# Kernel optimization log

Measured on AMD Instinct MI355X. Metric: run time of the kernel, lower is better.

Reference implementation:

```python
import jax, jax.numpy as jnp
import numpy as np

N_NODES = 100000
N_EDGES = 600000
HID = 128
N_ETYPES = 8


def setup_inputs() -> dict:
    key = jax.random.key(0)
    ks = jax.random.split(key, 10)
    s = 1.0 / np.sqrt(HID)
    return {
        "h": jax.random.normal(ks[0], (N_NODES, HID), dtype=jnp.float32),
        "edge_index": jax.random.randint(ks[1], (2, N_EDGES), 0, N_NODES, dtype=jnp.int64),
        "edge_type": jax.random.randint(ks[2], (N_EDGES,), 0, N_ETYPES, dtype=jnp.int64),
        # per-edge-type Linear(hidden, hidden): weight (T, H_out, H_in) stored as (T, H_in, H_out) for einsum
        "message_W": jax.random.uniform(ks[3], (N_ETYPES, HID, HID), jnp.float32, -s, s),
        "message_b": jax.random.uniform(ks[4], (N_ETYPES, HID), jnp.float32, -s, s),
        # GRUCell params (torch layout): w_ih (3H, H), w_hh (3H, H), b_ih (3H,), b_hh (3H,)
        "gru_w_ih": jax.random.uniform(ks[5], (3 * HID, HID), jnp.float32, -s, s),
        "gru_w_hh": jax.random.uniform(ks[6], (3 * HID, HID), jnp.float32, -s, s),
        "gru_b_ih": jax.random.uniform(ks[7], (3 * HID,), jnp.float32, -s, s),
        "gru_b_hh": jax.random.uniform(ks[8], (3 * HID,), jnp.float32, -s, s),
    }


def reference(h, edge_index, edge_type, message_W, message_b,
              gru_w_ih, gru_w_hh, gru_b_ih, gru_b_hh):
    num_nodes = h.shape[0]
    src, dst = edge_index[0], edge_index[1]

    # Transform every node by every edge-type Linear once: (N, T, H).
    # Equivalent to per-type msg = h[src] @ W[t].T + b[t] gathered by edge type.
    all_msgs = jnp.einsum('nh,thd->ntd', h, message_W) + message_b  # (N, T, H)
    msg = all_msgs[src, edge_type]                                   # (E, H) gather
    messages = jax.ops.segment_sum(msg, dst, num_segments=num_nodes)  # scatter-add

    # GRUCell: r,z,n gates (torch semantics)
    gi = messages @ gru_w_ih.T + gru_b_ih  # (N, 3H)
    gh = h @ gru_w_hh.T + gru_b_hh         # (N, 3H)
    i_r, i_z, i_n = jnp.split(gi, 3, axis=-1)
    h_r, h_z, h_n = jnp.split(gh, 3, axis=-1)
    r = jax.nn.sigmoid(i_r + h_r)
    z = jax.nn.sigmoid(i_z + h_z)
    n = jnp.tanh(i_n + r * h_n)
    return (1.0 - z) * n + z * h
```

## Files before the change

kernel.cpp:

```cpp
#include <hip/hip_runtime.h>

#define HID 128
#define NTY 8

typedef __attribute__((ext_vector_type(8))) short bf16x8;
typedef __attribute__((ext_vector_type(4))) float f32x4;

__device__ __forceinline__ unsigned short f2bf(float x) {
    unsigned u = __float_as_uint(x);
    u += 0x7FFF + ((u >> 16) & 1);
    return (unsigned short)(u >> 16);
}
__device__ __forceinline__ float bf2f(unsigned short s) {
    return __uint_as_float(((unsigned)s) << 16);
}
__device__ __forceinline__ float sigmoidf_fast(float x) {
    return 1.f / (1.f + __expf(-x));
}
__device__ __forceinline__ float tanhf_fast(float x) {
    return 1.f - 2.f / (1.f + __expf(2.f * x));
}

__global__ void conv_all_kernel(const float* __restrict__ h, unsigned short* __restrict__ hbf, int nh,
                                const float* __restrict__ W, unsigned short* __restrict__ wfr,
                                const float* __restrict__ wih, const float* __restrict__ whh,
                                unsigned short* __restrict__ wpkf,
                                int* __restrict__ sortedE, int capE,
                                int* __restrict__ seg8, int M8)
{
    int i = blockIdx.x * 256 + threadIdx.x;
    if (i < nh) { hbf[i] = f2bf(h[i]); return; }
    i -= nh;
    if (i < 131072) {
        int e = i & 7, lane = (i >> 3) & 63, cb = (i >> 9) & 7, kc = (i >> 12) & 3, t = i >> 14;
        int lr = lane & 15, quad = lane >> 4;
        int d = cb * 16 + lr;
        int k = kc * 32 + quad * 8 + e;
        wfr[i] = f2bf(W[(t << 14) + (k << 7) + d]);
        return;
    }
    i -= 131072;
    if (i < 98304) {
        int e = i & 7, lane = (i >> 3) & 63, f = i >> 9;
        int ct = f & 7, fg = f >> 3;
        int g3 = fg % 3, kc = fg / 3;
        int lr = lane & 15, quad = lane >> 4;
        int d = ct * 16 + lr;
        int kk = quad * 8 + e;
        float v;
        if (kc < 4) v = wih[(g3 * 128 + d) * 128 + kc * 32 + kk];
        else        v = whh[(g3 * 128 + d) * 128 + (kc - 4) * 32 + kk];
        wpkf[i] = f2bf(v);
        return;
    }
    i -= 98304;
    if (i < capE) { sortedE[i] = -1; return; }
    i -= capE;
    if (i < M8) seg8[i] = 0;
}

__global__ void hist8_kernel(const int* __restrict__ etype, const int* __restrict__ ei,
                             int E, int N, int* __restrict__ seg8) {
    int stride = gridDim.x * blockDim.x;
    for (int i = blockIdx.x * blockDim.x + threadIdx.x; i < E; i += stride)
        atomicAdd(&seg8[etype[i] * N + ei[E + i]], 1);
}

__global__ void scanA_kernel(int* __restrict__ seg8, int* __restrict__ bsum, int M8) {
    __shared__ int s[256];
    int i = blockIdx.x * 256 + threadIdx.x;
    int v = (i < M8) ? seg8[i] : 0;
    s[threadIdx.x] = v;
    __syncthreads();
    for (int off = 1; off < 256; off <<= 1) {
        int t = (threadIdx.x >= off) ? s[threadIdx.x - off] : 0;
        __syncthreads();
        s[threadIdx.x] += t;
        __syncthreads();
    }
    if (i < M8) seg8[i] = s[threadIdx.x] - v;
    if (threadIdx.x == 255) bsum[blockIdx.x] = s[255];
}

__global__ void scanBbig_kernel(int* __restrict__ bsum, int nb,
                                const int* __restrict__ seg8, int N, int E,
                                int* __restrict__ padB, int* __restrict__ padA) {
    __shared__ int s[256];
    int tx = threadIdx.x;
    int C = (nb + 255) / 256;
    int lo = tx * C, hi = lo + C; if (hi > nb) hi = nb;
    int sum = 0;
    for (int j = lo; j < hi; ++j) sum += bsum[j];
    s[tx] = sum;
    __syncthreads();
    for (int off = 1; off < 256; off <<= 1) {
        int t = (tx >= off) ? s[tx - off] : 0;
        __syncthreads();
        s[tx] += t;
        __syncthreads();
    }
    int run = s[tx] - sum;
    for (int j = lo; j < hi; ++j) { int v = bsum[j]; bsum[j] = run; run += v; }
    __syncthreads();
    if (tx == 0) {
        int r[9];
        for (int t = 0; t < 8; ++t) { int k = t * N; r[t] = seg8[k] + bsum[k >> 8]; }
        r[8] = E;
        int pb = 0;
        for (int t = 0; t < 8; ++t) {
            padB[t] = pb;
            padA[t] = pb - r[t];
            int c = r[t + 1] - r[t];
            pb += (c + 127) & ~127;
        }
        padB[8] = pb;
    }
}

__global__ void scanC_kernel(int* __restrict__ seg8, const int* __restrict__ bsum,
                             const int* __restrict__ padA, int M8, int N) {
    int i = blockIdx.x * 256 + threadIdx.x;
    if (i < M8) {
        int t = i / N;
        seg8[i] += bsum[i >> 8] + padA[t];
    }
}

__global__ void scatter8_kernel(const int* __restrict__ etype, const int* __restrict__ ei,
                                int E, int N, int* __restrict__ seg8, int* __restrict__ sortedE) {
    int stride = gridDim.x * blockDim.x;
    for (int i = blockIdx.x * blockDim.x + threadIdx.x; i < E; i += stride) {
        int pos = atomicAdd(&seg8[etype[i] * N + ei[E + i]], 1);
        sortedE[pos] = ei[i];
    }
}

__global__ __launch_bounds__(256) void msg_gemm(
    const unsigned short* __restrict__ hbf, const unsigned short* __restrict__ wfr,
    const float* __restrict__ bias, const int* __restrict__ sortedE,
    const int* __restrict__ padB, unsigned short* __restrict__ M)
{
    __shared__ unsigned short hs[128][136];
    __shared__ int srcs[128];
    __shared__ int stype;

    int tx = threadIdx.x;
    int base = blockIdx.x * 128;
    if (tx < 128) srcs[tx] = sortedE[base + tx];
    if (tx == 0) {
        int t = -1;
        #pragma unroll
        for (int tt = 0; tt < 8; ++tt)
            if (base >= padB[tt] && base < padB[tt + 1]) t = tt;
        stype = t;
    }
    __syncthreads();
    int t = stype;
    if (t < 0) return;

    for (int f = tx; f < 2048; f += 256) {
        int row = f >> 4, c8 = (f & 15) * 8;
        int s = srcs[row]; if (s < 0) s = 0;
        *(uint4*)&hs[row][c8] = *(const uint4*)&hbf[(size_t)s * 128 + c8];
    }
    __syncthreads();

    int lane = tx & 63, w = tx >> 6;
    int r0 = (w >> 1) * 64, c0 = (w & 1) * 64;
    int lr = lane & 15, quad = lane >> 4;
    f32x4 acc[4][4] = {};

    const unsigned short* wt = wfr + (t << 14) + ((unsigned)(c0 >> 4) << 9) + (lane << 3);
    #pragma unroll
    for (int kc = 0; kc < 4; ++kc) {
        bf16x8 af[4], wf[4];
        #pragma unroll
        for (int rb = 0; rb < 4; ++rb) af[rb] = *(const bf16x8*)&hs[r0 + rb * 16 + lr][kc * 32 + quad * 8];
        #pragma unroll
        for (int cb = 0; cb < 4; ++cb) wf[cb] = *(const bf16x8*)&wt[(kc << 12) + (cb << 9)];
        #pragma unroll
        for (int rb = 0; rb < 4; ++rb)
            #pragma unroll
            for (int cb = 0; cb < 4; ++cb)
                acc[rb][cb] = __builtin_amdgcn_mfma_f32_16x16x32_bf16(wf[cb], af[rb], acc[rb][cb], 0, 0, 0);
    }

    float4 bv4[4];
    #pragma unroll
    for (int cb = 0; cb < 4; ++cb)
        bv4[cb] = *(const float4*)&bias[t * 128 + c0 + cb * 16 + quad * 4];

    #pragma unroll
    for (int rb = 0; rb < 4; ++rb) {
        int e = r0 + rb * 16 + lr;
        size_t mrow = (size_t)(base + e);
        #pragma unroll
        for (int cb = 0; cb < 4; ++cb) {
            int d0 = c0 + cb * 16 + quad * 4;
            f32x4 a = acc[rb][cb];
            uint2 v;
            v.x = (unsigned)f2bf(a[0] + bv4[cb].x) | ((unsigned)f2bf(a[1] + bv4[cb].y) << 16);
            v.y = (unsigned)f2bf(a[2] + bv4[cb].z) | ((unsigned)f2bf(a[3] + bv4[cb].w) << 16);
            *(uint2*)&M[mrow * 128 + d0] = v;
        }
    }
}

__global__ __launch_bounds__(512, 4) void gru_fused(
    const unsigned short* __restrict__ M, const int* __restrict__ segE,
    const int* __restrict__ padB, const unsigned short* __restrict__ hbf,
    const unsigned short* __restrict__ wpkf, const float* __restrict__ bih,
    const float* __restrict__ bhh, const float* __restrict__ hf,
    float* __restrict__ out, int N)
{
    __shared__ unsigned short As[4][2048];
    __shared__ int bnds_l[520];

    int tx = threadIdx.x;
    int n0 = blockIdx.x * 64;

    for (int jl = tx; jl < 520; jl += 512) {
        int t = jl / 65, j = jl - t * 65;
        int nidx = n0 + j - 1;
        int v;
        if (nidx < 0) v = padB[t];
        else {
            if (nidx > N - 1) nidx = N - 1;
            v = segE[t * N + nidx];
        }
        bnds_l[jl] = v;
    }

    int lane = tx & 63, w = tx >> 6;
    int lr = lane & 15, quad = lane >> 4;
    int rt = w & 3, cg = w >> 2;
    int node = n0 + rt * 16 + lr;
    bool valid = node < N;
    int nc = valid ? node : (N - 1);

    bf16x8 afh[4];
    {
        const unsigned short* hrow = hbf + ((size_t)nc << 7) + (quad << 3);
        #pragma unroll
        for (int k4 = 0; k4 < 4; ++k4) afh[k4] = *(const bf16x8*)&hrow[k4 * 32];
    }
    __syncthreads();

    {
        int ln = tx >> 3, j8 = tx & 7;
        float a[16];
        #pragma unroll
        for (int j = 0; j < 16; ++j) a[j] = 0.f;

        int tcur = 0;
        int r = bnds_l[ln], re = bnds_l[ln + 1];
        while (r >= re && tcur < 7) {
            ++tcur;
            r = bnds_l[tcur * 65 + ln];
            re = bnds_l[tcur * 65 + ln + 1];
        }
        bool have = (r < re);
        uint4 c0v, c1v;
        if (have) {
            const unsigned short* p = M + (size_t)r * 128 + j8 * 16;
            c0v = *(const uint4*)p;
            c1v = *(const uint4*)(p + 8);
        }
        while (have) {
            uint4 p0 = c0v, p1 = c1v;
            int rn = r + 1, tn = tcur, ren = re;
            while (rn >= ren && tn < 7) {
                ++tn;
                rn = bnds_l[tn * 65 + ln];
                ren = bnds_l[tn * 65 + ln + 1];
            }
            bool haveN = (rn < ren);
            if (haveN) {
                const unsigned short* p = M + (size_t)rn * 128 + j8 * 16;
                c0v = *(const uint4*)p;
                c1v = *(const uint4*)(p + 8);
            }
            const unsigned short* q0 = (const unsigned short*)&p0;
            const unsigned short* q1 = (const unsigned short*)&p1;
            #pragma unroll
            for (int u = 0; u < 8; ++u) {
                a[u]     += bf2f(q0[u]);
                a[8 + u] += bf2f(q1[u]);
            }
            r = rn; tcur = tn; re = ren; have = haveN;
        }

        unsigned short tmp[16];
        #pragma unroll
        for (int j = 0; j < 16; ++j) tmp[j] = f2bf(a[j]);
        int lrw = ln & 15, wv = ln >> 4;
        int swz = (lrw & 7) << 4;
        int b0 = ((lrw << 8) + (j8 << 5)) ^ swz;
        int b1 = ((lrw << 8) + (j8 << 5) + 16) ^ swz;
        *(uint4*)((char*)&As[wv][0] + b0) = *(const uint4*)&tmp[0];
        *(uint4*)((char*)&As[wv][0] + b1) = *(const uint4*)&tmp[8];
    }
    __syncthreads();

    const unsigned short* AsW = &As[rt][0];
    const unsigned short* wg = wpkf + (lane << 3);

    f32x4 aR[4] = {}, aZ[4] = {}, aI[4] = {}, aH[4] = {};
    #pragma unroll
    for (int kc = 0; kc < 8; ++kc) {
        bf16x8 af;
        if (kc < 4) {
            int byte = ((lr << 8) + (kc << 6) + (quad << 4)) ^ ((lr & 7) << 4);
            af = *(const bf16x8*)((char*)AsW + byte);
        } else {
            af = afh[kc - 4];
        }
        #pragma unroll
        for (int g3 = 0; g3 < 3; ++g3) {
            #pragma unroll
            for (int ct = 0; ct < 4; ++ct) {
                bf16x8 wf = *(const bf16x8*)&wg[(unsigned)((kc * 3 + g3) * 8 + cg * 4 + ct) << 9];
                if (g3 == 0)      aR[ct] = __builtin_amdgcn_mfma_f32_16x16x32_bf16(wf, af, aR[ct], 0, 0, 0);
                else if (g3 == 1) aZ[ct] = __builtin_amdgcn_mfma_f32_16x16x32_bf16(wf, af, aZ[ct], 0, 0, 0);
                else if (kc < 4)  aI[ct] = __builtin_amdgcn_mfma_f32_16x16x32_bf16(wf, af, aI[ct], 0, 0, 0);
                else              aH[ct] = __builtin_amdgcn_mfma_f32_16x16x32_bf16(wf, af, aH[ct], 0, 0, 0);
            }
        }
    }

    if (valid) {
        #pragma unroll
        for (int ct = 0; ct < 4; ++ct) {
            int d0 = cg * 64 + ct * 16 + quad * 4;
            f32x4 bir = *(const f32x4*)&bih[d0],       bhr = *(const f32x4*)&bhh[d0];
            f32x4 biz = *(const f32x4*)&bih[128 + d0], bhz = *(const f32x4*)&bhh[128 + d0];
            f32x4 bin = *(const f32x4*)&bih[256 + d0], bhn = *(const f32x4*)&bhh[256 + d0];
            f32x4 h0 = *(const f32x4*)&hf[(size_t)node * 128 + d0];
            f32x4 o;
            #pragma unroll
            for (int j = 0; j < 4; ++j) {
                float r  = sigmoidf_fast(aR[ct][j] + bir[j] + bhr[j]);
                float z  = sigmoidf_fast(aZ[ct][j] + biz[j] + bhz[j]);
                float nn = tanhf_fast(aI[ct][j] + bin[j] + r * (aH[ct][j] + bhn[j]));
                o[j] = (1.f - z) * nn + z * h0[j];
            }
            *(f32x4*)&out[(size_t)node * 128 + d0] = o;
        }
    }
}

extern "C" void kernel_launch(void* const* d_in, const int* in_sizes, int n_in,
                              void* d_out, int out_size, void* d_ws, size_t ws_size,
                              hipStream_t stream)
{
    const float* h     = (const float*)d_in[0];
    const int*   ei    = (const int*)d_in[1];
    const int*   etype = (const int*)d_in[2];
    const float* W     = (const float*)d_in[3];
    const float* b     = (const float*)d_in[4];
    const float* wih   = (const float*)d_in[5];
    const float* whh   = (const float*)d_in[6];
    const float* bih   = (const float*)d_in[7];
    const float* bhh   = (const float*)d_in[8];
    float* out = (float*)d_out;

    int E = in_sizes[1] / 2;
    int N = in_sizes[0] / HID;
    int M8 = N * 8;
    int nbA = (M8 + 255) / 256;
    int capE = ((E + 127) / 128 + NTY) * 128;

    char* p = (char*)d_ws;
    auto alloc = [&](size_t bytes) { char* r = p; p += (bytes + 255) & ~(size_t)255; return r; };
    unsigned short* hbf  = (unsigned short*)alloc((size_t)N * 128 * 2);
    unsigned short* wfr  = (unsigned short*)alloc((size_t)131072 * 2);
    unsigned short* wpkf = (unsigned short*)alloc((size_t)98304 * 2);
    int* seg8    = (int*)alloc((size_t)M8 * 4);
    int* bsum    = (int*)alloc((size_t)nbA * 4);
    int* sortedE = (int*)alloc((size_t)capE * 4);
    int* padB    = (int*)alloc(9 * 4);
    int* padA    = (int*)alloc(8 * 4);
    unsigned short* M = (unsigned short*)alloc((size_t)capE * 128 * 2);
    (void)ws_size;

    int totalConv = N * 128 + 131072 + 98304 + capE + M8;
    conv_all_kernel<<<(totalConv + 255) / 256, 256, 0, stream>>>(
        h, hbf, N * 128, W, wfr, wih, whh, wpkf, sortedE, capE, seg8, M8);

    hist8_kernel<<<1024, 256, 0, stream>>>(etype, ei, E, N, seg8);
    scanA_kernel<<<nbA, 256, 0, stream>>>(seg8, bsum, M8);
    scanBbig_kernel<<<1, 256, 0, stream>>>(bsum, nbA, seg8, N, E, padB, padA);
    scanC_kernel<<<nbA, 256, 0, stream>>>(seg8, bsum, padA, M8, N);
    scatter8_kernel<<<1024, 256, 0, stream>>>(etype, ei, E, N, seg8, sortedE);

    msg_gemm<<<capE / 128, 256, 0, stream>>>(hbf, wfr, b, sortedE, padB, M);
    gru_fused<<<(N + 63) / 64, 512, 0, stream>>>(M, seg8, padB, hbf, wpkf, bih, bhh, h, out, N);
}
```

Measured before the change: 380.8 us.

## Fuse preprocessing and counting-sort stages into one cooperative kernel with grid syncs

```diff
diff --git a/kernel.cpp b/kernel.cpp
--- a/kernel.cpp
+++ b/kernel.cpp
@@ -1,4 +1,7 @@
 #include <hip/hip_runtime.h>
+#include <hip/hip_cooperative_groups.h>
+
+namespace cg = cooperative_groups;
 
 #define HID 128
 #define NTY 8
@@ -21,26 +24,35 @@
     return 1.f - 2.f / (1.f + __expf(2.f * x));
 }
 
-__global__ void conv_all_kernel(const float* __restrict__ h, unsigned short* __restrict__ hbf, int nh,
-                                const float* __restrict__ W, unsigned short* __restrict__ wfr,
-                                const float* __restrict__ wih, const float* __restrict__ whh,
-                                unsigned short* __restrict__ wpkf,
-                                int* __restrict__ sortedE, int capE,
-                                int* __restrict__ seg8, int M8)
+__global__ __launch_bounds__(256) void prep_sort_coop(
+    const float* __restrict__ h, unsigned short* __restrict__ hbf, int nh,
+    const float* __restrict__ W, unsigned short* __restrict__ wfr,
+    const float* __restrict__ wih, const float* __restrict__ whh,
+    unsigned short* __restrict__ wpkf,
+    const int* __restrict__ ei, const int* __restrict__ etype, int E, int N,
+    int* __restrict__ seg8, int* __restrict__ bsum,
+    int* __restrict__ padB, int* __restrict__ padA,
+    int* __restrict__ sortedE, int capE)
 {
-    int i = blockIdx.x * 256 + threadIdx.x;
-    if (i < nh) { hbf[i] = f2bf(h[i]); return; }
-    i -= nh;
-    if (i < 131072) {
+    cg::grid_group grid = cg::this_grid();
+    __shared__ int s[256];
+
+    int tx = threadIdx.x;
+    int gtid = blockIdx.x * 256 + tx;
+    int gsz = gridDim.x * 256;
+    int nb = gridDim.x;
+    int M8 = N * 8;
+    int CB = (M8 + nb - 1) / nb;
+
+    for (int i = gtid; i < nh; i += gsz) hbf[i] = f2bf(h[i]);
+    for (int i = gtid; i < 131072; i += gsz) {
         int e = i & 7, lane = (i >> 3) & 63, cb = (i >> 9) & 7, kc = (i >> 12) & 3, t = i >> 14;
         int lr = lane & 15, quad = lane >> 4;
         int d = cb * 16 + lr;
         int k = kc * 32 + quad * 8 + e;
         wfr[i] = f2bf(W[(t << 14) + (k << 7) + d]);
-        return;
-    }
-    i -= 131072;
-    if (i < 98304) {
+    }
+    for (int i = gtid; i < 98304; i += gsz) {
         int e = i & 7, lane = (i >> 3) & 63, f = i >> 9;
         int ct = f & 7, fg = f >> 3;
         int g3 = fg % 3, kc = fg / 3;
@@ -51,85 +63,78 @@
         if (kc < 4) v = wih[(g3 * 128 + d) * 128 + kc * 32 + kk];
         else        v = whh[(g3 * 128 + d) * 128 + (kc - 4) * 32 + kk];
         wpkf[i] = f2bf(v);
-        return;
-    }
-    i -= 98304;
-    if (i < capE) { sortedE[i] = -1; return; }
-    i -= capE;
-    if (i < M8) seg8[i] = 0;
-}
-
-__global__ void hist8_kernel(const int* __restrict__ etype, const int* __restrict__ ei,
-                             int E, int N, int* __restrict__ seg8) {
-    int stride = gridDim.x * blockDim.x;
-    for (int i = blockIdx.x * blockDim.x + threadIdx.x; i < E; i += stride)
+    }
+    for (int i = gtid; i < capE; i += gsz) sortedE[i] = -1;
+    for (int i = gtid; i < M8; i += gsz) seg8[i] = 0;
+    grid.sync();
+
+    for (int i = gtid; i < E; i += gsz)
         atomicAdd(&seg8[etype[i] * N + ei[E + i]], 1);
-}
-
-__global__ void scanA_kernel(int* __restrict__ seg8, int* __restrict__ bsum, int M8) {
-    __shared__ int s[256];
-    int i = blockIdx.x * 256 + threadIdx.x;
-    int v = (i < M8) ? seg8[i] : 0;
-    s[threadIdx.x] = v;
-    __syncthreads();
-    for (int off = 1; off < 256; off <<= 1) {
-        int t = (threadIdx.x >= off) ? s[threadIdx.x - off] : 0;
+    grid.sync();
+
+    {
+        int b0 = blockIdx.x * CB;
+        int bend = b0 + CB; if (bend > M8) bend = M8;
+        int cpt = (CB + 255) / 256;
+        int t0 = b0 + tx * cpt;
+        int t1 = t0 + cpt; if (t1 > bend) t1 = bend;
+        int sum = 0;
+        for (int k = t0; k < t1; ++k) sum += seg8[k];
+        s[tx] = sum;
         __syncthreads();
-        s[threadIdx.x] += t;
+        for (int off = 1; off < 256; off <<= 1) {
+            int t = (tx >= off) ? s[tx - off] : 0;
+            __syncthreads();
+            s[tx] += t;
+            __syncthreads();
+        }
+        int run = s[tx] - sum;
+        for (int k = t0; k < t1; ++k) { int v = seg8[k]; seg8[k] = run; run += v; }
+        if (tx == 255) bsum[blockIdx.x] = s[255];
+    }
+    grid.sync();
+
+    if (blockIdx.x == 0) {
+        int cpt = (nb + 255) / 256;
+        int t0 = tx * cpt;
+        int t1 = t0 + cpt; if (t1 > nb) t1 = nb;
+        int sum = 0;
+        for (int k = t0; k < t1; ++k) sum += bsum[k];
+        s[tx] = sum;
         __syncthreads();
-    }
-    if (i < M8) seg8[i] = s[threadIdx.x] - v;
-    if (threadIdx.x == 255) bsum[blockIdx.x] = s[255];
-}
-
-__global__ void scanBbig_kernel(int* __restrict__ bsum, int nb,
-                                const int* __restrict__ seg8, int N, int E,
-                                int* __restrict__ padB, int* __restrict__ padA) {
-    __shared__ int s[256];
-    int tx = threadIdx.x;
-    int C = (nb + 255) / 256;
-    int lo = tx * C, hi = lo + C; if (hi > nb) hi = nb;
-    int sum = 0;
-    for (int j = lo; j < hi; ++j) sum += bsum[j];
-    s[tx] = sum;
-    __syncthreads();
-    for (int off = 1; off < 256; off <<= 1) {
-        int t = (tx >= off) ? s[tx - off] : 0;
+        for (int off = 1; off < 256; off <<= 1) {
+            int t = (tx >= off) ? s[tx - off] : 0;
+            __syncthreads();
+            s[tx] += t;
+            __syncthreads();
+        }
+        int run = s[tx] - sum;
+        for (int k = t0; k < t1; ++k) { int v = bsum[k]; bsum[k] = run; run += v; }
         __syncthreads();
-        s[tx] += t;
-        __syncthreads();
-    }
-    int run = s[tx] - sum;
-    for (int j = lo; j < hi; ++j) { int v = bsum[j]; bsum[j] = run; run += v; }
-    __syncthreads();
-    if (tx == 0) {
-        int r[9];
-        for (int t = 0; t < 8; ++t) { int k = t * N; r[t] = seg8[k] + bsum[k >> 8]; }
-        r[8] = E;
-        int pb = 0;
-        for (int t = 0; t < 8; ++t) {
-            padB[t] = pb;
-            padA[t] = pb - r[t];
-            int c = r[t + 1] - r[t];
-            pb += (c + 127) & ~127;
-        }
-        padB[8] = pb;
-    }
-}
-
-__global__ void scanC_kernel(int* __restrict__ seg8, const int* __restrict__ bsum,
-                             const int* __restrict__ padA, int M8, int N) {
-    int i = blockIdx.x * 256 + threadIdx.x;
-    if (i < M8) {
-        int t = i / N;
-        seg8[i] += bsum[i >> 8] + padA[t];
-    }
-}
-
-__global__ void scatter8_kernel(const int* __restrict__ etype, const int* __restrict__ ei,
-                                int E, int N, int* __restrict__ seg8, int* __restrict__ sortedE) {
-    int stride = gridDim.x * blockDim.x;
-    for (int i = blockIdx.x * blockDim.x + threadIdx.x; i < E; i += stride) {
+        if (tx == 0) {
+            int r[9];
+            for (int t = 0; t < 8; ++t) {
+                int k = t * N;
+                r[t] = seg8[k] + bsum[k / CB];
+            }
+            r[8] = E;
+            int pb = 0;
+            for (int t = 0; t < 8; ++t) {
+                padB[t] = pb;
+                padA[t] = pb - r[t];
+                int c = r[t + 1] - r[t];
+                pb += (c + 127) & ~127;
+            }
+            padB[8] = pb;
+        }
+    }
+    grid.sync();
+
+    for (int i = gtid; i < M8; i += gsz)
+        seg8[i] += bsum[i / CB] + padA[i / N];
+    grid.sync();
+
+    for (int i = gtid; i < E; i += gsz) {
         int pos = atomicAdd(&seg8[etype[i] * N + ei[E + i]], 1);
         sortedE[pos] = ei[i];
     }
@@ -367,31 +372,32 @@
     int E = in_sizes[1] / 2;
     int N = in_sizes[0] / HID;
     int M8 = N * 8;
-    int nbA = (M8 + 255) / 256;
     int capE = ((E + 127) / 128 + NTY) * 128;
+    int nh = N * 128;
 
     char* p = (char*)d_ws;
     auto alloc = [&](size_t bytes) { char* r = p; p += (bytes + 255) & ~(size_t)255; return r; };
-    unsigned short* hbf  = (unsigned short*)alloc((size_t)N * 128 * 2);
+    unsigned short* hbf  = (unsigned short*)alloc((size_t)nh * 2);
     unsigned short* wfr  = (unsigned short*)alloc((size_t)131072 * 2);
     unsigned short* wpkf = (unsigned short*)alloc((size_t)98304 * 2);
     int* seg8    = (int*)alloc((size_t)M8 * 4);
-    int* bsum    = (int*)alloc((size_t)nbA * 4);
+    int* bsum    = (int*)alloc(1024 * 4);
     int* sortedE = (int*)alloc((size_t)capE * 4);
     int* padB    = (int*)alloc(9 * 4);
     int* padA    = (int*)alloc(8 * 4);
     unsigned short* M = (unsigned short*)alloc((size_t)capE * 128 * 2);
     (void)ws_size;
 
-    int totalConv = N * 128 + 131072 + 98304 + capE + M8;
-    conv_all_kernel<<<(totalConv + 255) / 256, 256, 0, stream>>>(
-        h, hbf, N * 128, W, wfr, wih, whh, wpkf, sortedE, capE, seg8, M8);
-
-    hist8_kernel<<<1024, 256, 0, stream>>>(etype, ei, E, N, seg8);
-    scanA_kernel<<<nbA, 256, 0, stream>>>(seg8, bsum, M8);
-    scanBbig_kernel<<<1, 256, 0, stream>>>(bsum, nbA, seg8, N, E, padB, padA);
-    scanC_kernel<<<nbA, 256, 0, stream>>>(seg8, bsum, padA, M8, N);
-    scatter8_kernel<<<1024, 256, 0, stream>>>(etype, ei, E, N, seg8, sortedE);
+    void* args[] = {
+        (void*)&h, (void*)&hbf, (void*)&nh,
+        (void*)&W, (void*)&wfr,
+        (void*)&wih, (void*)&whh, (void*)&wpkf,
+        (void*)&ei, (void*)&etype, (void*)&E, (void*)&N,
+        (void*)&seg8, (void*)&bsum, (void*)&padB, (void*)&padA,
+        (void*)&sortedE, (void*)&capE
+    };
+    hipLaunchCooperativeKernel((const void*)prep_sort_coop,
+                               dim3(1024), dim3(256), args, 0, stream);
 
     msg_gemm<<<capE / 128, 256, 0, stream>>>(hbf, wfr, b, sortedE, padB, M);
     gru_fused<<<(N + 63) / 64, 512, 0, stream>>>(M, seg8, padB, hbf, wpkf, bih, bhh, h, out, N);
```

After: 923.4 us. 142% more time.

## Fuse histogram into conversion kernel, drop scanC pass, and interleave segment gathers

Applied to the files above, without the earlier changes.

```diff
diff --git a/kernel.cpp b/kernel.cpp
--- a/kernel.cpp
+++ b/kernel.cpp
@@ -21,26 +21,26 @@
     return 1.f - 2.f / (1.f + __expf(2.f * x));
 }
 
-__global__ void conv_all_kernel(const float* __restrict__ h, unsigned short* __restrict__ hbf, int nh,
-                                const float* __restrict__ W, unsigned short* __restrict__ wfr,
-                                const float* __restrict__ wih, const float* __restrict__ whh,
-                                unsigned short* __restrict__ wpkf,
-                                int* __restrict__ sortedE, int capE,
-                                int* __restrict__ seg8, int M8)
+__global__ __launch_bounds__(256) void conv_hist(
+    const float* __restrict__ h, unsigned short* __restrict__ hbf, int nh,
+    const float* __restrict__ W, unsigned short* __restrict__ wfr,
+    const float* __restrict__ wih, const float* __restrict__ whh,
+    unsigned short* __restrict__ wpkf,
+    const int* __restrict__ ei, const int* __restrict__ etype, int E, int N,
+    int* __restrict__ seg8)
 {
-    int i = blockIdx.x * 256 + threadIdx.x;
-    if (i < nh) { hbf[i] = f2bf(h[i]); return; }
-    i -= nh;
-    if (i < 131072) {
+    int gtid = blockIdx.x * 256 + threadIdx.x;
+    int gsz = gridDim.x * 256;
+
+    for (int i = gtid; i < nh; i += gsz) hbf[i] = f2bf(h[i]);
+    for (int i = gtid; i < 131072; i += gsz) {
         int e = i & 7, lane = (i >> 3) & 63, cb = (i >> 9) & 7, kc = (i >> 12) & 3, t = i >> 14;
         int lr = lane & 15, quad = lane >> 4;
         int d = cb * 16 + lr;
         int k = kc * 32 + quad * 8 + e;
         wfr[i] = f2bf(W[(t << 14) + (k << 7) + d]);
-        return;
-    }
-    i -= 131072;
-    if (i < 98304) {
+    }
+    for (int i = gtid; i < 98304; i += gsz) {
         int e = i & 7, lane = (i >> 3) & 63, f = i >> 9;
         int ct = f & 7, fg = f >> 3;
         int g3 = fg % 3, kc = fg / 3;
@@ -51,18 +51,8 @@
         if (kc < 4) v = wih[(g3 * 128 + d) * 128 + kc * 32 + kk];
         else        v = whh[(g3 * 128 + d) * 128 + (kc - 4) * 32 + kk];
         wpkf[i] = f2bf(v);
-        return;
-    }
-    i -= 98304;
-    if (i < capE) { sortedE[i] = -1; return; }
-    i -= capE;
-    if (i < M8) seg8[i] = 0;
-}
-
-__global__ void hist8_kernel(const int* __restrict__ etype, const int* __restrict__ ei,
-                             int E, int N, int* __restrict__ seg8) {
-    int stride = gridDim.x * blockDim.x;
-    for (int i = blockIdx.x * blockDim.x + threadIdx.x; i < E; i += stride)
+    }
+    for (int i = gtid; i < E; i += gsz)
         atomicAdd(&seg8[etype[i] * N + ei[E + i]], 1);
 }
 
@@ -84,7 +74,8 @@
 
 __global__ void scanBbig_kernel(int* __restrict__ bsum, int nb,
                                 const int* __restrict__ seg8, int N, int E,
-                                int* __restrict__ padB, int* __restrict__ padA) {
+                                int* __restrict__ padB, int* __restrict__ padA,
+                                int* __restrict__ trueE) {
     __shared__ int s[256];
     int tx = threadIdx.x;
     int C = (nb + 255) / 256;
@@ -111,56 +102,56 @@
             padB[t] = pb;
             padA[t] = pb - r[t];
             int c = r[t + 1] - r[t];
+            trueE[t] = pb + c;
             pb += (c + 127) & ~127;
         }
         padB[8] = pb;
     }
 }
 
-__global__ void scanC_kernel(int* __restrict__ seg8, const int* __restrict__ bsum,
-                             const int* __restrict__ padA, int M8, int N) {
-    int i = blockIdx.x * 256 + threadIdx.x;
-    if (i < M8) {
-        int t = i / N;
-        seg8[i] += bsum[i >> 8] + padA[t];
-    }
-}
-
 __global__ void scatter8_kernel(const int* __restrict__ etype, const int* __restrict__ ei,
-                                int E, int N, int* __restrict__ seg8, int* __restrict__ sortedE) {
+                                int E, int N, int* __restrict__ seg8,
+                                const int* __restrict__ bsum, const int* __restrict__ padA,
+                                int* __restrict__ sortedE) {
     int stride = gridDim.x * blockDim.x;
     for (int i = blockIdx.x * blockDim.x + threadIdx.x; i < E; i += stride) {
-        int pos = atomicAdd(&seg8[etype[i] * N + ei[E + i]], 1);
-        sortedE[pos] = ei[i];
+        int t = etype[i];
+        int k = t * N + ei[E + i];
+        int lp = atomicAdd(&seg8[k], 1);
+        sortedE[lp + bsum[k >> 8] + padA[t]] = ei[i];
     }
 }
 
 __global__ __launch_bounds__(256) void msg_gemm(
     const unsigned short* __restrict__ hbf, const unsigned short* __restrict__ wfr,
     const float* __restrict__ bias, const int* __restrict__ sortedE,
-    const int* __restrict__ padB, unsigned short* __restrict__ M)
+    const int* __restrict__ padB, const int* __restrict__ trueE,
+    unsigned short* __restrict__ M)
 {
     __shared__ unsigned short hs[128][136];
     __shared__ int srcs[128];
-    __shared__ int stype;
+    __shared__ int stype, send;
 
     int tx = threadIdx.x;
     int base = blockIdx.x * 128;
-    if (tx < 128) srcs[tx] = sortedE[base + tx];
     if (tx == 0) {
         int t = -1;
         #pragma unroll
         for (int tt = 0; tt < 8; ++tt)
             if (base >= padB[tt] && base < padB[tt + 1]) t = tt;
         stype = t;
+        send = (t >= 0) ? trueE[t] : 0;
     }
     __syncthreads();
     int t = stype;
     if (t < 0) return;
+    int sEnd = send;
+    if (tx < 128) srcs[tx] = (base + tx < sEnd) ? sortedE[base + tx] : 0;
+    __syncthreads();
 
     for (int f = tx; f < 2048; f += 256) {
         int row = f >> 4, c8 = (f & 15) * 8;
-        int s = srcs[row]; if (s < 0) s = 0;
+        int s = srcs[row];
         *(uint4*)&hs[row][c8] = *(const uint4*)&hbf[(size_t)s * 128 + c8];
     }
     __syncthreads();
@@ -208,6 +199,7 @@
 
 __global__ __launch_bounds__(512, 4) void gru_fused(
     const unsigned short* __restrict__ M, const int* __restrict__ segE,
+    const int* __restrict__ bsum, const int* __restrict__ padA,
     const int* __restrict__ padB, const unsigned short* __restrict__ hbf,
     const unsigned short* __restrict__ wpkf, const float* __restrict__ bih,
     const float* __restrict__ bhh, const float* __restrict__ hf,
@@ -226,7 +218,8 @@
         if (nidx < 0) v = padB[t];
         else {
             if (nidx > N - 1) nidx = N - 1;
-            v = segE[t * N + nidx];
+            int k = t * N + nidx;
+            v = segE[k] + bsum[k >> 8] + padA[t];
         }
         bnds_l[jl] = v;
     }
@@ -252,42 +245,54 @@
         #pragma unroll
         for (int j = 0; j < 16; ++j) a[j] = 0.f;
 
-        int tcur = 0;
-        int r = bnds_l[ln], re = bnds_l[ln + 1];
-        while (r >= re && tcur < 7) {
-            ++tcur;
-            r = bnds_l[tcur * 65 + ln];
-            re = bnds_l[tcur * 65 + ln + 1];
-        }
-        bool have = (r < re);
-        uint4 c0v, c1v;
-        if (have) {
-            const unsigned short* p = M + (size_t)r * 128 + j8 * 16;
-            c0v = *(const uint4*)p;
-            c1v = *(const uint4*)(p + 8);
-        }
-        while (have) {
-            uint4 p0 = c0v, p1 = c1v;
-            int rn = r + 1, tn = tcur, ren = re;
-            while (rn >= ren && tn < 7) {
-                ++tn;
-                rn = bnds_l[tn * 65 + ln];
-                ren = bnds_l[tn * 65 + ln + 1];
+        int rr[4], ree[4], tc[4];
+        bool hv[4];
+        uint4 pb0[4], pb1[4];
+        #pragma unroll
+        for (int c = 0; c < 4; ++c) {
+            int t0 = 2 * c;
+            int r = bnds_l[t0 * 65 + ln], re = bnds_l[t0 * 65 + ln + 1];
+            int tcc = t0;
+            if (r >= re) {
+                tcc = t0 + 1;
+                r = bnds_l[tcc * 65 + ln];
+                re = bnds_l[tcc * 65 + ln + 1];
             }
-            bool haveN = (rn < ren);
-            if (haveN) {
-                const unsigned short* p = M + (size_t)rn * 128 + j8 * 16;
-                c0v = *(const uint4*)p;
-                c1v = *(const uint4*)(p + 8);
+            hv[c] = (r < re);
+            rr[c] = r; ree[c] = re; tc[c] = tcc;
+            if (hv[c]) {
+                const unsigned short* p = M + (size_t)r * 128 + j8 * 16;
+                pb0[c] = *(const uint4*)p;
+                pb1[c] = *(const uint4*)(p + 8);
             }
-            const unsigned short* q0 = (const unsigned short*)&p0;
-            const unsigned short* q1 = (const unsigned short*)&p1;
+        }
+        while (hv[0] | hv[1] | hv[2] | hv[3]) {
             #pragma unroll
-            for (int u = 0; u < 8; ++u) {
-                a[u]     += bf2f(q0[u]);
-                a[8 + u] += bf2f(q1[u]);
+            for (int c = 0; c < 4; ++c) {
+                if (hv[c]) {
+                    uint4 p0 = pb0[c], p1 = pb1[c];
+                    int rn = rr[c] + 1, tn = tc[c], ren = ree[c];
+                    if (rn >= ren && tn == 2 * c) {
+                        tn = 2 * c + 1;
+                        rn = bnds_l[tn * 65 + ln];
+                        ren = bnds_l[tn * 65 + ln + 1];
+                    }
+                    bool hN = (rn < ren);
+                    if (hN) {
+                        const unsigned short* p = M + (size_t)rn * 128 + j8 * 16;
+                        pb0[c] = *(const uint4*)p;
+                        pb1[c] = *(const uint4*)(p + 8);
+                    }
+                    const unsigned short* q0 = (const unsigned short*)&p0;
+                    const unsigned short* q1 = (const unsigned short*)&p1;
+                    #pragma unroll
+                    for (int u = 0; u < 8; ++u) {
+                        a[u]     += bf2f(q0[u]);
+                        a[8 + u] += bf2f(q1[u]);
+                    }
+                    rr[c] = rn; tc[c] = tn; ree[c] = ren; hv[c] = hN;
+                }
             }
-            r = rn; tcur = tn; re = ren; have = haveN;
         }
 
         unsigned short tmp[16];
@@ -369,10 +374,11 @@
     int M8 = N * 8;
     int nbA = (M8 + 255) / 256;
     int capE = ((E + 127) / 128 + NTY) * 128;
+    int nh = N * 128;
 
     char* p = (char*)d_ws;
     auto alloc = [&](size_t bytes) { char* r = p; p += (bytes + 255) & ~(size_t)255; return r; };
-    unsigned short* hbf  = (unsigned short*)alloc((size_t)N * 128 * 2);
+    unsigned short* hbf  = (unsigned short*)alloc((size_t)nh * 2);
     unsigned short* wfr  = (unsigned short*)alloc((size_t)131072 * 2);
     unsigned short* wpkf = (unsigned short*)alloc((size_t)98304 * 2);
     int* seg8    = (int*)alloc((size_t)M8 * 4);
@@ -380,19 +386,19 @@
     int* sortedE = (int*)alloc((size_t)capE * 4);
     int* padB    = (int*)alloc(9 * 4);
     int* padA    = (int*)alloc(8 * 4);
+    int* trueE   = (int*)alloc(8 * 4);
     unsigned short* M = (unsigned short*)alloc((size_t)capE * 128 * 2);
     (void)ws_size;
 
-    int totalConv = N * 128 + 131072 + 98304 + capE + M8;
-    conv_all_kernel<<<(totalConv + 255) / 256, 256, 0, stream>>>(
-        h, hbf, N * 128, W, wfr, wih, whh, wpkf, sortedE, capE, seg8, M8);
-
-    hist8_kernel<<<1024, 256, 0, stream>>>(etype, ei, E, N, seg8);
+    hipMemsetAsync(seg8, 0, (size_t)M8 * 4, stream);
+
+    conv_hist<<<2048, 256, 0, stream>>>(h, hbf, nh, W, wfr, wih, whh, wpkf,
+                                        ei, etype, E, N, seg8);
     scanA_kernel<<<nbA, 256, 0, stream>>>(seg8, bsum, M8);
-    scanBbig_kernel<<<1, 256, 0, stream>>>(bsum, nbA, seg8, N, E, padB, padA);
-    scanC_kernel<<<nbA, 256, 0, stream>>>(seg8, bsum, padA, M8, N);
-    scatter8_kernel<<<1024, 256, 0, stream>>>(etype, ei, E, N, seg8, sortedE);
-
-    msg_gemm<<<capE / 128, 256, 0, stream>>>(hbf, wfr, b, sortedE, padB, M);
-    gru_fused<<<(N + 63) / 64, 512, 0, stream>>>(M, seg8, padB, hbf, wpkf, bih, bhh, h, out, N);
-}
+    scanBbig_kernel<<<1, 256, 0, stream>>>(bsum, nbA, seg8, N, E, padB, padA, trueE);
+    scatter8_kernel<<<1024, 256, 0, stream>>>(etype, ei, E, N, seg8, bsum, padA, sortedE);
+
+    msg_gemm<<<capE / 128, 256, 0, stream>>>(hbf, wfr, b, sortedE, padB, trueE, M);
+    gru_fused<<<(N + 63) / 64, 512, 0, stream>>>(M, seg8, bsum, padA, padB, hbf, wpkf,
+                                                 bih, bhh, h, out, N);
+}
```

Result: faster. 357.8 us (-6.0%).
